# Optimization experiments

Measured on AMD Instinct MI355X. Metric: run time of the kernel, lower is better.

## Reference

```python
import jax, jax.numpy as jnp
import numpy as np

N_NODES = 50000
N_EDGES = 800000


def spmm(edge_src, edge_dst, edge_weight, h):
    # out[i] = sum over edges (src->dst=i) of w * h[src]  == adj @ h
    msgs = h[edge_src] * edge_weight[:, None]  # [E, D]
    return jax.ops.segment_sum(msgs, edge_dst, num_segments=N_NODES)


def setup_inputs() -> dict:
    key = jax.random.key(0)
    ks = jax.random.split(key, 12)
    x = jax.random.normal(ks[0], (N_NODES, 512), dtype=jnp.float32)
    edge_src = jax.random.randint(ks[1], (N_EDGES,), 0, N_NODES, dtype=jnp.int32)
    edge_dst = jax.random.randint(ks[2], (N_EDGES,), 0, N_NODES, dtype=jnp.int32)
    edge_weight = jax.random.uniform(ks[3], (N_EDGES,), dtype=jnp.float32)
    def init_w(k, fin, fout):
        s = 1.0 / np.sqrt(fout)
        return jax.random.uniform(k, (fin, fout), minval=-s, maxval=s, dtype=jnp.float32)
    W1 = init_w(ks[4], 512, 512); b1 = jnp.zeros((512,), jnp.float32)
    W2 = init_w(ks[5], 512, 256); b2 = jnp.zeros((256,), jnp.float32)
    W3 = init_w(ks[6], 256, 128); b3 = jnp.zeros((128,), jnp.float32)
    W4 = init_w(ks[7], 128, 64);  b4 = jnp.zeros((64,), jnp.float32)
    return {"x": x, "edge_src": edge_src, "edge_dst": edge_dst,
            "edge_weight": edge_weight, "W1": W1, "b1": b1, "W2": W2,
            "b2": b2, "W3": W3, "b3": b3, "W4": W4, "b4": b4}


def reference(x, edge_src, edge_dst, edge_weight, W1, b1, W2, b2, W3, b3, W4, b4):
    # GraphConvolution: out = adj @ (x @ W) + b ; dropout is identity in eval mode
    def gc(h, W, b):
        return spmm(edge_src, edge_dst, edge_weight, h @ W) + b
    h = jax.nn.relu(gc(x, W1, b1))
    h = jax.nn.relu(gc(h, W2, b2))
    h = jax.nn.relu(gc(h, W3, b3))
    emb = gc(h, W4, b4)
    return emb
```

## Files before the change

kernel.cpp:

```cpp
#include <hip/hip_runtime.h>

#define NN 50000
#define NE 800000
#define SCAN_BLOCKS 196

typedef __attribute__((ext_vector_type(8))) short short8;
typedef __attribute__((ext_vector_type(4))) float float4v;

struct us4 { unsigned short x, y, z, w; };
struct us8 { unsigned short v[8]; };

__device__ __forceinline__ unsigned short f2bf(float f) {
    unsigned u = __float_as_uint(f);
    unsigned r = (u + 0x7FFF + ((u >> 16) & 1)) >> 16;
    return (unsigned short)r;
}

__device__ __forceinline__ float bf2f(unsigned short u) {
    return __uint_as_float((unsigned)u << 16);
}

__device__ __forceinline__ void gload_lds16(const unsigned short* g, unsigned short* l) {
    __builtin_amdgcn_global_load_lds(
        (const __attribute__((address_space(1))) unsigned int*)g,
        (__attribute__((address_space(3))) unsigned int*)l,
        16, 0, 0);
}

template <int BM, int BN, int WM, int WN, int OUTBF>
__global__ __launch_bounds__(256) void gemm_mfma(const unsigned short* __restrict__ A,
                                                 const unsigned short* __restrict__ Bt,
                                                 void* __restrict__ Cv,
                                                 int N, int K, int M) {
    constexpr int BK = 32;
    constexpr int MT = WM / 16;
    constexpr int NT = WN / 16;
    constexpr int WCOLS = BN / WN;

    __shared__ __align__(16) unsigned short As[BM * BK];
    __shared__ __align__(16) unsigned short Bs[BN * BK];

    const int tid = threadIdx.x;
    const int lane = tid & 63;
    const int wid = tid >> 6;
    const int col16 = lane & 15;
    const int q = lane >> 4;
    const int wr = (wid / WCOLS) * WM;
    const int wc = (wid % WCOLS) * WN;
    const int rowBase = blockIdx.y * BM;
    const int colBase = blockIdx.x * BN;

    const int srow = lane >> 2;
    const int scol = (lane & 3) * 8;

    float4v acc[MT][NT];
#pragma unroll
    for (int t = 0; t < MT; ++t)
#pragma unroll
        for (int u = 0; u < NT; ++u)
            acc[t][u] = (float4v)0.f;

    for (int k0 = 0; k0 < K; k0 += BK) {
        __syncthreads();
#pragma unroll
        for (int l = wid; l < BM / 16; l += 4) {
            int row = rowBase + 16 * l + srow;
            row = row < N ? row : N - 1;
            gload_lds16(A + (size_t)row * K + k0 + scol, &As[l * 512]);
        }
#pragma unroll
        for (int l = wid; l < BN / 16; l += 4) {
            const int row = colBase + 16 * l + srow;
            gload_lds16(Bt + (size_t)row * K + k0 + scol, &Bs[l * 512]);
        }
        __syncthreads();

        short8 a[MT], b[NT];
#pragma unroll
        for (int t = 0; t < MT; ++t)
            a[t] = *(const short8*)&As[(wr + t * 16 + col16) * BK + q * 8];
#pragma unroll
        for (int u = 0; u < NT; ++u)
            b[u] = *(const short8*)&Bs[(wc + u * 16 + col16) * BK + q * 8];
#pragma unroll
        for (int t = 0; t < MT; ++t)
#pragma unroll
            for (int u = 0; u < NT; ++u)
                acc[t][u] = __builtin_amdgcn_mfma_f32_16x16x32_bf16(a[t], b[u], acc[t][u], 0, 0, 0);
    }

#pragma unroll
    for (int t = 0; t < MT; ++t) {
        const int row0 = rowBase + wr + t * 16 + q * 4;
#pragma unroll
        for (int u = 0; u < NT; ++u) {
            const int col = colBase + wc + u * 16 + col16;
#pragma unroll
            for (int r = 0; r < 4; ++r) {
                const int row = row0 + r;
                if (row < N) {
                    if (OUTBF)
                        ((unsigned short*)Cv)[(size_t)row * M + col] = f2bf(acc[t][u][r]);
                    else
                        ((float*)Cv)[(size_t)row * M + col] = acc[t][u][r];
                }
            }
        }
    }
}

__global__ void cvt_f32_bf16(const float* __restrict__ in, unsigned short* __restrict__ out,
                             long long n4) {
    long long i = (long long)blockIdx.x * blockDim.x + threadIdx.x;
    const long long stride = (long long)gridDim.x * blockDim.x;
    for (; i < n4; i += stride) {
        const float4 v = *(const float4*)&in[i * 4];
        us4 o = {f2bf(v.x), f2bf(v.y), f2bf(v.z), f2bf(v.w)};
        *(us4*)&out[i * 4] = o;
    }
}

__global__ void cvt_transpose_all(const float* __restrict__ W1, unsigned short* __restrict__ Wt1,
                                  const float* __restrict__ W2, unsigned short* __restrict__ Wt2,
                                  const float* __restrict__ W3, unsigned short* __restrict__ Wt3,
                                  const float* __restrict__ W4, unsigned short* __restrict__ Wt4) {
    int idx = blockIdx.x * blockDim.x + threadIdx.x;
    const float* W; unsigned short* Wt; int K, M;
    if (idx < 262144)      { W = W1; Wt = Wt1; K = 512; M = 512; }
    else if (idx < 393216) { idx -= 262144; W = W2; Wt = Wt2; K = 512; M = 256; }
    else if (idx < 425984) { idx -= 393216; W = W3; Wt = Wt3; K = 256; M = 128; }
    else if (idx < 434176) { idx -= 425984; W = W4; Wt = Wt4; K = 128; M = 64; }
    else return;
    const int k = idx / M;
    const int m = idx % M;
    Wt[(size_t)m * K + k] = f2bf(W[(size_t)k * M + m]);
}

__global__ void zero_counts(int* __restrict__ counts) {
    int i = blockIdx.x * blockDim.x + threadIdx.x;
    if (i < NN) counts[i] = 0;
}

__global__ void hist_dst(const int* __restrict__ dst, int* __restrict__ counts) {
    int i = blockIdx.x * blockDim.x + threadIdx.x;
    const int stride = gridDim.x * blockDim.x;
    for (; i < NE; i += stride) atomicAdd(&counts[dst[i]], 1);
}

__global__ __launch_bounds__(256) void scan_partial(const int* __restrict__ counts,
                                                    int* __restrict__ partials) {
    __shared__ int r[256];
    const int t = threadIdx.x;
    const int i = blockIdx.x * 256 + t;
    r[t] = (i < NN) ? counts[i] : 0;
    __syncthreads();
    for (int s = 128; s > 0; s >>= 1) {
        if (t < s) r[t] += r[t + s];
        __syncthreads();
    }
    if (t == 0) partials[blockIdx.x] = r[0];
}

__global__ __launch_bounds__(256) void scan_base(const int* __restrict__ partials,
                                                 int* __restrict__ bases,
                                                 int* __restrict__ offs) {
    __shared__ int s[256];
    const int t = threadIdx.x;
    const int v = (t < SCAN_BLOCKS) ? partials[t] : 0;
    s[t] = v;
    __syncthreads();
    for (int off = 1; off < 256; off <<= 1) {
        int x = (t >= off) ? s[t - off] : 0;
        __syncthreads();
        s[t] += x;
        __syncthreads();
    }
    if (t < SCAN_BLOCKS) bases[t] = s[t] - v;
    if (t == 255) offs[NN] = s[255];
}

__global__ __launch_bounds__(256) void scan_final(int* __restrict__ counts,
                                                  const int* __restrict__ bases,
                                                  int* __restrict__ offs) {
    __shared__ int s[256];
    const int t = threadIdx.x;
    const int i = blockIdx.x * 256 + t;
    const int v = (i < NN) ? counts[i] : 0;
    s[t] = v;
    __syncthreads();
    for (int off = 1; off < 256; off <<= 1) {
        int x = (t >= off) ? s[t - off] : 0;
        __syncthreads();
        s[t] += x;
        __syncthreads();
    }
    if (i < NN) {
        const int e = bases[blockIdx.x] + s[t] - v;
        offs[i] = e;
        counts[i] = e;
    }
}

__global__ void fill_csr(const int* __restrict__ src, const int* __restrict__ dst,
                         const float* __restrict__ w, int* __restrict__ cursor,
                         int* __restrict__ csr_src, float* __restrict__ csr_w) {
    int i = blockIdx.x * blockDim.x + threadIdx.x;
    const int stride = gridDim.x * blockDim.x;
    for (; i < NE; i += stride) {
        const int p = atomicAdd(&cursor[dst[i]], 1);
        csr_src[p] = src[i];
        csr_w[p] = w[i];
    }
}

template <int D, int RELU, int OUTBF>
__global__ __launch_bounds__(256) void spmm_gather(const int* __restrict__ offs,
                                                   const int* __restrict__ csr_src,
                                                   const float* __restrict__ csr_w,
                                                   const unsigned short* __restrict__ hp,
                                                   const float* __restrict__ bias,
                                                   void* __restrict__ outv,
                                                   int dbase, int dstride) {
    constexpr int TPN = D / 8;
    constexpr int NPB = 256 / TPN;
    const int tid = threadIdx.x;
    const int node = blockIdx.x * NPB + tid / TPN;
    const int d = dbase + (tid % TPN) * 8;
    if (node >= NN) return;
    const int beg = offs[node];
    const int end = offs[node + 1];

    float acc[8] = {};
    int j = beg;
    for (; j + 4 <= end; j += 4) {
        const int s0 = csr_src[j];
        const int s1 = csr_src[j + 1];
        const int s2 = csr_src[j + 2];
        const int s3 = csr_src[j + 3];
        const float w0 = csr_w[j];
        const float w1 = csr_w[j + 1];
        const float w2 = csr_w[j + 2];
        const float w3 = csr_w[j + 3];
        const us8 h0 = *(const us8*)&hp[(long long)s0 * dstride + d];
        const us8 h1 = *(const us8*)&hp[(long long)s1 * dstride + d];
        const us8 h2 = *(const us8*)&hp[(long long)s2 * dstride + d];
        const us8 h3 = *(const us8*)&hp[(long long)s3 * dstride + d];
#pragma unroll
        for (int k = 0; k < 8; ++k)
            acc[k] += w0 * bf2f(h0.v[k]) + w1 * bf2f(h1.v[k])
                    + w2 * bf2f(h2.v[k]) + w3 * bf2f(h3.v[k]);
    }
    for (; j < end; ++j) {
        const int s0 = csr_src[j];
        const float w0 = csr_w[j];
        const us8 h0 = *(const us8*)&hp[(long long)s0 * dstride + d];
#pragma unroll
        for (int k = 0; k < 8; ++k)
            acc[k] += w0 * bf2f(h0.v[k]);
    }
#pragma unroll
    for (int k = 0; k < 8; ++k) {
        acc[k] += bias[d + k];
        if (RELU) acc[k] = fmaxf(acc[k], 0.f);
    }
    if (OUTBF) {
        us8 o;
#pragma unroll
        for (int k = 0; k < 8; ++k) o.v[k] = f2bf(acc[k]);
        *(us8*)((unsigned short*)outv + (long long)node * dstride + d) = o;
    } else {
        float* op = (float*)outv + (long long)node * dstride + d;
        *(float4*)op = make_float4(acc[0], acc[1], acc[2], acc[3]);
        *(float4*)(op + 4) = make_float4(acc[4], acc[5], acc[6], acc[7]);
    }
}

extern "C" void kernel_launch(void* const* d_in, const int* in_sizes, int n_in,
                              void* d_out, int out_size, void* d_ws, size_t ws_size,
                              hipStream_t stream) {
    const float* x    = (const float*)d_in[0];
    const int*   esrc = (const int*)d_in[1];
    const int*   edst = (const int*)d_in[2];
    const float* ew   = (const float*)d_in[3];
    const float* W1 = (const float*)d_in[4];  const float* b1 = (const float*)d_in[5];
    const float* W2 = (const float*)d_in[6];  const float* b2 = (const float*)d_in[7];
    const float* W3 = (const float*)d_in[8];  const float* b3 = (const float*)d_in[9];
    const float* W4 = (const float*)d_in[10]; const float* b4 = (const float*)d_in[11];
    float* out = (float*)d_out;

    char* ws = (char*)d_ws;
    int*   offs    = (int*)ws;                    ws += (NN + 1) * sizeof(int);
    int*   counts  = (int*)ws;                    ws += NN * sizeof(int);
    int*   partials= (int*)ws;                    ws += 256 * sizeof(int);
    int*   bases   = (int*)ws;                    ws += 256 * sizeof(int);
    int*   csr_src = (int*)ws;                    ws += NE * sizeof(int);
    float* csr_w   = (float*)ws;                  ws += NE * sizeof(float);
    unsigned short* Wt1 = (unsigned short*)ws;    ws += 512 * 512 * sizeof(unsigned short);
    unsigned short* Wt2 = (unsigned short*)ws;    ws += 256 * 512 * sizeof(unsigned short);
    unsigned short* Wt3 = (unsigned short*)ws;    ws += 128 * 256 * sizeof(unsigned short);
    unsigned short* Wt4 = (unsigned short*)ws;    ws += 64 * 128 * sizeof(unsigned short);
    ws = (char*)(((uintptr_t)ws + 255) & ~(uintptr_t)255);
    unsigned short* tmp = (unsigned short*)ws;    ws += (size_t)NN * 512 * sizeof(unsigned short);
    ws = (char*)(((uintptr_t)ws + 255) & ~(uintptr_t)255);
    unsigned short* hb = (unsigned short*)ws;

    zero_counts<<<(NN + 255) / 256, 256, 0, stream>>>(counts);
    hist_dst<<<3125, 256, 0, stream>>>(edst, counts);
    scan_partial<<<SCAN_BLOCKS, 256, 0, stream>>>(counts, partials);
    scan_base<<<1, 256, 0, stream>>>(partials, bases, offs);
    scan_final<<<SCAN_BLOCKS, 256, 0, stream>>>(counts, bases, offs);
    fill_csr<<<3125, 256, 0, stream>>>(esrc, edst, ew, counts, csr_src, csr_w);

    cvt_f32_bf16<<<12800, 256, 0, stream>>>(x, hb, (long long)NN * 512 / 4);
    cvt_transpose_all<<<(434176 + 255) / 256, 256, 0, stream>>>(W1, Wt1, W2, Wt2, W3, Wt3, W4, Wt4);

    const int nby128 = (NN + 127) / 128;
    const int nby64  = (NN + 63) / 64;

    gemm_mfma<128, 128, 64, 64, 1><<<dim3(4, nby128), 256, 0, stream>>>(hb, Wt1, tmp, NN, 512, 512);
    spmm_gather<256, 1, 1><<<NN / 8, 256, 0, stream>>>(offs, csr_src, csr_w, tmp, b1, hb, 0, 512);
    spmm_gather<256, 1, 1><<<NN / 8, 256, 0, stream>>>(offs, csr_src, csr_w, tmp, b1, hb, 256, 512);
    gemm_mfma<128, 128, 64, 64, 1><<<dim3(2, nby128), 256, 0, stream>>>(hb, Wt2, tmp, NN, 512, 256);
    spmm_gather<256, 1, 1><<<NN / 8, 256, 0, stream>>>(offs, csr_src, csr_w, tmp, b2, hb, 0, 256);
    gemm_mfma<64, 128, 32, 64, 1><<<dim3(1, nby64), 256, 0, stream>>>(hb, Wt3, tmp, NN, 256, 128);
    spmm_gather<128, 1, 1><<<NN / 16, 256, 0, stream>>>(offs, csr_src, csr_w, tmp, b3, hb, 0, 128);
    gemm_mfma<64, 64, 32, 32, 1><<<dim3(1, nby64), 256, 0, stream>>>(hb, Wt4, tmp, NN, 128, 64);
    spmm_gather<64, 0, 0><<<(NN + 31) / 32, 256, 0, stream>>>(offs, csr_src, csr_w, tmp, b4, out, 0, 64);
}
```

Baseline: 609.6 us.

## Use full-width GEMM tiles with 512 threads and pack CSR edges as int2

The GEMM now uses 512-thread blocks whose tile spans all output columns, so each block reads its A rows exactly once instead of once per column tile. A and B tile loads are spread over all eight waves. Separately, the CSR source index and weight are interleaved into one int2 array, so the SpMM gather does one 8-byte load per edge instead of two 4-byte loads from separate arrays. The risks are larger shared-memory footprints and more accumulator registers per wave (e.g. a 32x128 warp tile in layer 1), which can lower occupancy.

```diff
diff --git a/kernel.cpp b/kernel.cpp
--- a/kernel.cpp
+++ b/kernel.cpp
@@ -28,14 +28,17 @@
 }
 
 template <int BM, int BN, int WM, int WN, int OUTBF>
-__global__ __launch_bounds__(256) void gemm_mfma(const unsigned short* __restrict__ A,
-                                                 const unsigned short* __restrict__ Bt,
-                                                 void* __restrict__ Cv,
-                                                 int N, int K, int M) {
+__global__ __launch_bounds__(512) void gemm_mfma2(const unsigned short* __restrict__ A,
+                                                  const unsigned short* __restrict__ Bt,
+                                                  void* __restrict__ Cv,
+                                                  int N, int K, int M) {
     constexpr int BK = 32;
     constexpr int MT = WM / 16;
     constexpr int NT = WN / 16;
     constexpr int WCOLS = BN / WN;
+    constexpr int NWAVES = (BM / WM) * WCOLS;
+    constexpr int ACH = BM / 16;
+    constexpr int BCH = BN / 16;
 
     __shared__ __align__(16) unsigned short As[BM * BK];
     __shared__ __align__(16) unsigned short Bs[BN * BK];
@@ -47,8 +50,7 @@
     const int q = lane >> 4;
     const int wr = (wid / WCOLS) * WM;
     const int wc = (wid % WCOLS) * WN;
-    const int rowBase = blockIdx.y * BM;
-    const int colBase = blockIdx.x * BN;
+    const int rowBase = blockIdx.x * BM;
 
     const int srow = lane >> 2;
     const int scol = (lane & 3) * 8;
@@ -63,15 +65,16 @@
     for (int k0 = 0; k0 < K; k0 += BK) {
         __syncthreads();
 #pragma unroll
-        for (int l = wid; l < BM / 16; l += 4) {
-            int row = rowBase + 16 * l + srow;
-            row = row < N ? row : N - 1;
-            gload_lds16(A + (size_t)row * K + k0 + scol, &As[l * 512]);
-        }
-#pragma unroll
-        for (int l = wid; l < BN / 16; l += 4) {
-            const int row = colBase + 16 * l + srow;
-            gload_lds16(Bt + (size_t)row * K + k0 + scol, &Bs[l * 512]);
+        for (int l = wid; l < ACH + BCH; l += NWAVES) {
+            if (l < ACH) {
+                int row = rowBase + 16 * l + srow;
+                row = row < N ? row : N - 1;
+                gload_lds16(A + (size_t)row * K + k0 + scol, &As[l * 512]);
+            } else {
+                const int lb = l - ACH;
+                const int brow = 16 * lb + srow;
+                gload_lds16(Bt + (size_t)brow * K + k0 + scol, &Bs[lb * 512]);
+            }
         }
         __syncthreads();
 
@@ -94,7 +97,7 @@
         const int row0 = rowBase + wr + t * 16 + q * 4;
 #pragma unroll
         for (int u = 0; u < NT; ++u) {
-            const int col = colBase + wc + u * 16 + col16;
+            const int col = wc + u * 16 + col16;
 #pragma unroll
             for (int r = 0; r < 4; ++r) {
                 const int row = row0 + r;
@@ -203,20 +206,18 @@
 
 __global__ void fill_csr(const int* __restrict__ src, const int* __restrict__ dst,
                          const float* __restrict__ w, int* __restrict__ cursor,
-                         int* __restrict__ csr_src, float* __restrict__ csr_w) {
+                         int2* __restrict__ csr_e) {
     int i = blockIdx.x * blockDim.x + threadIdx.x;
     const int stride = gridDim.x * blockDim.x;
     for (; i < NE; i += stride) {
         const int p = atomicAdd(&cursor[dst[i]], 1);
-        csr_src[p] = src[i];
-        csr_w[p] = w[i];
+        csr_e[p] = make_int2(src[i], __float_as_int(w[i]));
     }
 }
 
 template <int D, int RELU, int OUTBF>
 __global__ __launch_bounds__(256) void spmm_gather(const int* __restrict__ offs,
-                                                   const int* __restrict__ csr_src,
-                                                   const float* __restrict__ csr_w,
+                                                   const int2* __restrict__ csr_e,
                                                    const unsigned short* __restrict__ hp,
                                                    const float* __restrict__ bias,
                                                    void* __restrict__ outv,
@@ -233,27 +234,27 @@
     float acc[8] = {};
     int j = beg;
     for (; j + 4 <= end; j += 4) {
-        const int s0 = csr_src[j];
-        const int s1 = csr_src[j + 1];
-        const int s2 = csr_src[j + 2];
-        const int s3 = csr_src[j + 3];
-        const float w0 = csr_w[j];
-        const float w1 = csr_w[j + 1];
-        const float w2 = csr_w[j + 2];
-        const float w3 = csr_w[j + 3];
-        const us8 h0 = *(const us8*)&hp[(long long)s0 * dstride + d];
-        const us8 h1 = *(const us8*)&hp[(long long)s1 * dstride + d];
-        const us8 h2 = *(const us8*)&hp[(long long)s2 * dstride + d];
-        const us8 h3 = *(const us8*)&hp[(long long)s3 * dstride + d];
+        const int2 e0 = csr_e[j];
+        const int2 e1 = csr_e[j + 1];
+        const int2 e2 = csr_e[j + 2];
+        const int2 e3 = csr_e[j + 3];
+        const float w0 = __int_as_float(e0.y);
+        const float w1 = __int_as_float(e1.y);
+        const float w2 = __int_as_float(e2.y);
+        const float w3 = __int_as_float(e3.y);
+        const us8 h0 = *(const us8*)&hp[(long long)e0.x * dstride + d];
+        const us8 h1 = *(const us8*)&hp[(long long)e1.x * dstride + d];
+        const us8 h2 = *(const us8*)&hp[(long long)e2.x * dstride + d];
+        const us8 h3 = *(const us8*)&hp[(long long)e3.x * dstride + d];
 #pragma unroll
         for (int k = 0; k < 8; ++k)
             acc[k] += w0 * bf2f(h0.v[k]) + w1 * bf2f(h1.v[k])
                     + w2 * bf2f(h2.v[k]) + w3 * bf2f(h3.v[k]);
     }
     for (; j < end; ++j) {
-        const int s0 = csr_src[j];
-        const float w0 = csr_w[j];
-        const us8 h0 = *(const us8*)&hp[(long long)s0 * dstride + d];
+        const int2 e0 = csr_e[j];
+        const float w0 = __int_as_float(e0.y);
+        const us8 h0 = *(const us8*)&hp[(long long)e0.x * dstride + d];
 #pragma unroll
         for (int k = 0; k < 8; ++k)
             acc[k] += w0 * bf2f(h0.v[k]);
@@ -293,8 +294,8 @@
     int*   counts  = (int*)ws;                    ws += NN * sizeof(int);
     int*   partials= (int*)ws;                    ws += 256 * sizeof(int);
     int*   bases   = (int*)ws;                    ws += 256 * sizeof(int);
-    int*   csr_src = (int*)ws;                    ws += NE * sizeof(int);
-    float* csr_w   = (float*)ws;                  ws += NE * sizeof(float);
+    ws = (char*)(((uintptr_t)ws + 255) & ~(uintptr_t)255);
+    int2*  csr_e   = (int2*)ws;                   ws += (size_t)NE * sizeof(int2);
     unsigned short* Wt1 = (unsigned short*)ws;    ws += 512 * 512 * sizeof(unsigned short);
     unsigned short* Wt2 = (unsigned short*)ws;    ws += 256 * 512 * sizeof(unsigned short);
     unsigned short* Wt3 = (unsigned short*)ws;    ws += 128 * 256 * sizeof(unsigned short);
@@ -309,21 +310,20 @@
     scan_partial<<<SCAN_BLOCKS, 256, 0, stream>>>(counts, partials);
     scan_base<<<1, 256, 0, stream>>>(partials, bases, offs);
     scan_final<<<SCAN_BLOCKS, 256, 0, stream>>>(counts, bases, offs);
-    fill_csr<<<3125, 256, 0, stream>>>(esrc, edst, ew, counts, csr_src, csr_w);
+    fill_csr<<<3125, 256, 0, stream>>>(esrc, edst, ew, counts, csr_e);
 
     cvt_f32_bf16<<<12800, 256, 0, stream>>>(x, hb, (long long)NN * 512 / 4);
     cvt_transpose_all<<<(434176 + 255) / 256, 256, 0, stream>>>(W1, Wt1, W2, Wt2, W3, Wt3, W4, Wt4);
 
-    const int nby128 = (NN + 127) / 128;
-    const int nby64  = (NN + 63) / 64;
-
-    gemm_mfma<128, 128, 64, 64, 1><<<dim3(4, nby128), 256, 0, stream>>>(hb, Wt1, tmp, NN, 512, 512);
-    spmm_gather<256, 1, 1><<<NN / 8, 256, 0, stream>>>(offs, csr_src, csr_w, tmp, b1, hb, 0, 512);
-    spmm_gather<256, 1, 1><<<NN / 8, 256, 0, stream>>>(offs, csr_src, csr_w, tmp, b1, hb, 256, 512);
-    gemm_mfma<128, 128, 64, 64, 1><<<dim3(2, nby128), 256, 0, stream>>>(hb, Wt2, tmp, NN, 512, 256);
-    spmm_gather<256, 1, 1><<<NN / 8, 256, 0, stream>>>(offs, csr_src, csr_w, tmp, b2, hb, 0, 256);
-    gemm_mfma<64, 128, 32, 64, 1><<<dim3(1, nby64), 256, 0, stream>>>(hb, Wt3, tmp, NN, 256, 128);
-    spmm_gather<128, 1, 1><<<NN / 16, 256, 0, stream>>>(offs, csr_src, csr_w, tmp, b3, hb, 0, 128);
-    gemm_mfma<64, 64, 32, 32, 1><<<dim3(1, nby64), 256, 0, stream>>>(hb, Wt4, tmp, NN, 128, 64);
-    spmm_gather<64, 0, 0><<<(NN + 31) / 32, 256, 0, stream>>>(offs, csr_src, csr_w, tmp, b4, out, 0, 64);
-}
+    const int nbx = (NN + 63) / 64;
+
+    gemm_mfma2<64, 512, 32, 128, 1><<<nbx, 512, 0, stream>>>(hb, Wt1, tmp, NN, 512, 512);
+    spmm_gather<256, 1, 1><<<NN / 8, 256, 0, stream>>>(offs, csr_e, tmp, b1, hb, 0, 512);
+    spmm_gather<256, 1, 1><<<NN / 8, 256, 0, stream>>>(offs, csr_e, tmp, b1, hb, 256, 512);
+    gemm_mfma2<64, 256, 32, 64, 1><<<nbx, 512, 0, stream>>>(hb, Wt2, tmp, NN, 512, 256);
+    spmm_gather<256, 1, 1><<<NN / 8, 256, 0, stream>>>(offs, csr_e, tmp, b2, hb, 0, 256);
+    gemm_mfma2<64, 128, 32, 32, 1><<<nbx, 512, 0, stream>>>(hb, Wt3, tmp, NN, 256, 128);
+    spmm_gather<128, 1, 1><<<NN / 16, 256, 0, stream>>>(offs, csr_e, tmp, b3, hb, 0, 128);
+    gemm_mfma2<64, 64, 32, 16, 1><<<nbx, 512, 0, stream>>>(hb, Wt4, tmp, NN, 128, 64);
+    spmm_gather<64, 0, 0><<<(NN + 31) / 32, 256, 0, stream>>>(offs, csr_e, tmp, b4, out, 0, 64);
+}
```

Result: slower. 632.8 us (+3.8%).
